# Optimization experiments

Measured on AMD Instinct MI355X. Metric: run time of the kernel, lower is better.

The kernel has to match this reference:

```python
import jax, jax.numpy as jnp
import numpy as np

START = 5.0
STEP = 8
SIZE = 256
STOP = SIZE // 2 - 1.0  # self.stop = int(size/2) - 1.0
# Original loops over tf.linspace(s, stop, step) and truncates each value to int.
US = [int(v) for v in np.linspace(START, STOP, STEP)]


def _block_mask(w, h, u):
    # Boolean block of ones of size (2u+1)^2 centered at (w//2, h//2).
    # Original: dd[half_w-u:half_w+u+1, half_h-u:half_h+u+1] = 1, then keeps
    # only that region of the shifted spectrum (ideal low-pass filter).
    m = np.zeros((w, h), dtype=np.float32)
    m[w // 2 - u: w // 2 + u + 1, h // 2 - u: h // 2 + u + 1] = 1.0
    return jnp.asarray(m)


def setup_inputs() -> dict:
    key = jax.random.key(0)
    x = jax.random.normal(key, (64, SIZE, SIZE, 1), dtype=jnp.float32)
    return {"x": x}


def reference(x):
    n, w, h, c = x.shape  # c == 1
    im = x[..., 0].astype(jnp.complex64)  # [n, w, h]
    # FFT is identical across loop iterations in the original; hoist it.
    # fftshift/ifftshift over all axes in TF cancel on the batch axis, so
    # shifting only the spatial axes is mathematically identical.
    freq = jnp.fft.fftshift(jnp.fft.fft2(im), axes=(-2, -1))
    outs = [x]
    for u in US:  # small fixed loop over STEP cutoff radii
        mask = _block_mask(w, h, u)
        low = freq * mask.astype(jnp.complex64)  # keep low frequencies only
        out = jnp.real(jnp.fft.ifft2(jnp.fft.ifftshift(low, axes=(-2, -1))))
        outs.append(out.astype(x.dtype)[..., None])
    return jnp.concatenate(outs, axis=-1)  # [n, w, h, STEP+1]
```

## Files before the change

kernel.cpp:

```cpp
#include <hip/hip_runtime.h>

typedef __attribute__((ext_vector_type(4))) float          f32x4;
typedef __attribute__((ext_vector_type(2))) float          f32x2;
typedef __attribute__((ext_vector_type(4))) unsigned int   u32x4;
typedef __attribute__((ext_vector_type(4))) unsigned short u16x4;
typedef __attribute__((ext_vector_type(2))) unsigned short u16x2;

typedef const unsigned int __attribute__((address_space(1)))* gas_ptr;
typedef unsigned int __attribute__((address_space(3)))*       las_ptr;

#define PI_F 3.14159265358979f

__device__ __forceinline__ unsigned short f2bf(float f) {
    unsigned int x = __float_as_uint(f);
    unsigned int r = ((x >> 16) & 1u) + 0x7fffu;
    return (unsigned short)((x + r) >> 16);
}
__device__ __forceinline__ float bf2f(unsigned short v) {
    return __uint_as_float((unsigned int)v << 16);
}
__device__ __forceinline__ void mfma16(f32x4& c, u32x4 a, u32x4 b) {
    asm volatile("v_mfma_f32_16x16x32_bf16 %0, %1, %2, %0"
                 : "+v"(c) : "v"(a), "v"(b));
}
__device__ __forceinline__ void gload16(const void* g, void* l) {
    __builtin_amdgcn_global_load_lds((gas_ptr)g, (las_ptr)l, 16, 0, 0);
}

#define SWZ(r, cb) (((unsigned)(r) * 128u) + ((unsigned)(cb) ^ ((((unsigned)(r)) & 7u) << 4)))

__global__ void prep(const float* __restrict__ x, unsigned short* __restrict__ H,
                     unsigned short* __restrict__ Xb, float* __restrict__ out,
                     int write_c0) {
    int b = blockIdx.x;
    if (b < 2048) {
        const int US[8] = {5, 22, 39, 57, 74, 92, 109, 127};
        int idx = b * 256 + threadIdx.x;
        int u = idx >> 16;
        int i = (idx >> 8) & 255, js = idx & 255;
        int jl = js ^ ((i & 7) << 3);
        int d = (i - jl) & 255;
        int m = 2 * US[u] + 1;
        float h;
        if (d == 0) {
            h = (float)m * (1.0f / 256.0f);
        } else {
            int t = (m * d) & 511;
            float num = sinf((float)t * (PI_F / 256.0f));
            float den = sinf((float)d * (PI_F / 256.0f));
            h = num / (256.0f * den);
        }
        H[idx] = f2bf(h);
    } else {
        int idx = (b - 2048) * 256 + threadIdx.x;
        f32x4 v = ((const f32x4*)x)[idx];
        u16x4 o = { f2bf(v.x), f2bf(v.y), f2bf(v.z), f2bf(v.w) };
        int n = idx >> 14;
        int t = idx & 16383;
        int i = t >> 6;
        int jlin = (t & 63) * 4;
        int js = jlin ^ ((i & 7) << 3);
        *(u16x4*)(Xb + (size_t)n * 65536 + i * 256 + js) = o;
        if (write_c0) {
            size_t g = (size_t)idx * 4;
            out[(g + 0) * 9] = v.x;
            out[(g + 1) * 9] = v.y;
            out[(g + 2) * 9] = v.z;
            out[(g + 3) * 9] = v.w;
        }
    }
}

__global__ void __launch_bounds__(256) stage12(const unsigned short* __restrict__ Xb,
                                               const unsigned short* __restrict__ H,
                                               unsigned short* __restrict__ Zb,
                                               float* __restrict__ fOut,
                                               int mode, int u_fixed) {
    extern __shared__ char smem[];
    char* sStage = smem;
    char* sHq    = smem + 32768;
    char* sT     = smem + 40960;

    int n, u, jq;
    if (u_fixed >= 0) {
        n = blockIdx.x >> 2; jq = blockIdx.x & 3; u = u_fixed;
    } else {
        int swz = (blockIdx.x & 7) * 256 + (blockIdx.x >> 3);
        n = swz >> 5; u = (swz >> 2) & 7; jq = swz & 3;
    }

    const char* Xn = (const char*)(Xb + (size_t)n * 65536);
    const char* Hu = (const char*)(H + (size_t)u * 65536);

    const int tid  = threadIdx.x;
    const int lane = tid & 63;
    const int w    = tid >> 6;
    const int lrow = lane & 15;
    const int lk   = lane >> 4;
    const int srow = lane >> 3, sch = lane & 7;

    f32x4 acc[4][4];
#pragma unroll
    for (int a = 0; a < 4; ++a)
#pragma unroll
        for (int b = 0; b < 4; ++b) acc[a][b] = (f32x4){0.f, 0.f, 0.f, 0.f};

    for (int kt = 0; kt < 4; ++kt) {
        if (kt) __syncthreads();
#pragma unroll
        for (int q = 0; q < 8; ++q) {
            int r = (w * 8 + q) * 8 + srow;
            gload16(Xn + r * 512 + kt * 128 + sch * 16, sStage + (w * 8 + q) * 1024);
        }
#pragma unroll
        for (int q = 0; q < 2; ++q) {
            int r = jq * 64 + (w * 2 + q) * 8 + srow;
            gload16(Hu + r * 512 + kt * 128 + sch * 16, sHq + (w * 2 + q) * 1024);
        }
        __syncthreads();
#pragma unroll
        for (int kk = 0; kk < 2; ++kk) {
            const int kb = kk * 64 + lk * 16;
            u32x4 af[4], bf[4];
#pragma unroll
            for (int mi = 0; mi < 4; ++mi)
                af[mi] = *(const u32x4*)(sStage + SWZ(w * 64 + mi * 16 + lrow, kb));
#pragma unroll
            for (int ni = 0; ni < 4; ++ni)
                bf[ni] = *(const u32x4*)(sHq + SWZ(ni * 16 + lrow, kb));
#pragma unroll
            for (int mi = 0; mi < 4; ++mi)
#pragma unroll
                for (int ni = 0; ni < 4; ++ni)
                    mfma16(acc[mi][ni], af[mi], bf[ni]);
        }
    }
    asm volatile("s_nop 7\n\ts_nop 7");

#pragma unroll
    for (int mi = 0; mi < 4; ++mi) {
        int i4 = w * 64 + mi * 16 + (lane >> 4) * 4;
#pragma unroll
        for (int ni = 0; ni < 4; ++ni) {
            int jl = ni * 16 + lrow;
            u16x4 o = { f2bf(acc[mi][ni].x), f2bf(acc[mi][ni].y),
                        f2bf(acc[mi][ni].z), f2bf(acc[mi][ni].w) };
            *(u16x4*)(sT + jl * 512 + ((2 * i4) ^ ((jl & 7) << 4))) = o;
        }
    }
    __syncthreads();

#pragma unroll
    for (int a = 0; a < 4; ++a)
#pragma unroll
        for (int b = 0; b < 4; ++b) acc[a][b] = (f32x4){0.f, 0.f, 0.f, 0.f};

    for (int kt = 0; kt < 4; ++kt) {
        if (kt) __syncthreads();
#pragma unroll
        for (int q = 0; q < 8; ++q) {
            int r = (w * 8 + q) * 8 + srow;
            gload16(Hu + r * 512 + kt * 128 + sch * 16, sStage + (w * 8 + q) * 1024);
        }
        __syncthreads();
#pragma unroll
        for (int kk = 0; kk < 2; ++kk) {
            const int kb  = kk * 64 + lk * 16;
            const int kbT = kt * 128 + kb;
            u32x4 af[4], bf[4];
#pragma unroll
            for (int mi = 0; mi < 4; ++mi) {
                int r = mi * 16 + lrow;
                af[mi] = *(const u32x4*)(sT + r * 512 + (kbT ^ ((r & 7) << 4)));
            }
#pragma unroll
            for (int ni = 0; ni < 4; ++ni)
                bf[ni] = *(const u32x4*)(sStage + SWZ(w * 64 + ni * 16 + lrow, kb));
#pragma unroll
            for (int mi = 0; mi < 4; ++mi)
#pragma unroll
                for (int ni = 0; ni < 4; ++ni)
                    mfma16(acc[mi][ni], af[mi], bf[ni]);
        }
    }
    asm volatile("s_nop 7\n\ts_nop 7");

    if (mode == 0) {
        unsigned short* Op = Zb + ((size_t)(u * 64 + n)) * 65536 + jq * 64;
#pragma unroll
        for (int mi = 0; mi < 4; ++mi) {
            int r4 = mi * 16 + (lane >> 4) * 4;
#pragma unroll
            for (int ni = 0; ni < 4; ++ni) {
                int c = w * 64 + ni * 16 + lrow;
                u16x4 o = { f2bf(acc[mi][ni].x), f2bf(acc[mi][ni].y),
                            f2bf(acc[mi][ni].z), f2bf(acc[mi][ni].w) };
                *(u16x4*)(Op + (size_t)c * 256 + r4) = o;
            }
        }
    } else {
#pragma unroll
        for (int mi = 0; mi < 4; ++mi) {
            int r4 = mi * 16 + (lane >> 4) * 4;
#pragma unroll
            for (int ni = 0; ni < 4; ++ni) {
                int c = w * 64 + ni * 16 + lrow;
                float* o = fOut + (((size_t)n * 256 + c) * 256 + jq * 64 + r4) * 9 + 1 + u;
                o[0]  = acc[mi][ni].x;
                o[9]  = acc[mi][ni].y;
                o[18] = acc[mi][ni].z;
                o[27] = acc[mi][ni].w;
            }
        }
    }
}

__global__ void __launch_bounds__(256) pack9(const float* __restrict__ x,
                                             const unsigned short* __restrict__ Zb,
                                             float* __restrict__ out) {
    __shared__ float sl[9216];
    const int t = threadIdx.x;
    const size_t g0 = (size_t)blockIdx.x * 1024;

#pragma unroll
    for (int c = 0; c < 2; ++c) {
        int q = c * 512 + t * 2;
        size_t p = g0 + q;
        f32x2 xv = *(const f32x2*)(x + p);
        sl[q * 9]       = xv.x;
        sl[(q + 1) * 9] = xv.y;
#pragma unroll
        for (int u = 0; u < 8; ++u) {
            u16x2 z = *(const u16x2*)(Zb + (size_t)u * 4194304 + p);
            sl[q * 9 + 1 + u]       = bf2f(z.x);
            sl[(q + 1) * 9 + 1 + u] = bf2f(z.y);
        }
    }
    __syncthreads();
    float* ob = out + g0 * 9;
#pragma unroll
    for (int r = 0; r < 9; ++r) {
        int d = r * 1024 + t * 4;
        *(f32x4*)(ob + d) = *(const f32x4*)&sl[d];
    }
}

extern "C" void kernel_launch(void* const* d_in, const int* in_sizes, int n_in,
                              void* d_out, int out_size, void* d_ws, size_t ws_size,
                              hipStream_t stream) {
    const float* x = (const float*)d_in[0];
    float* out = (float*)d_out;
    char* ws = (char*)d_ws;

    unsigned short* H  = (unsigned short*)(ws);
    unsigned short* Xb = (unsigned short*)(ws + 1048576);
    unsigned short* Zb = (unsigned short*)(ws + 9437184);

    const size_t NEED_FULL = 76546048ull;
    const size_t LDS_BYTES = 73728;

    if (ws_size >= NEED_FULL) {
        prep<<<6144, 256, 0, stream>>>(x, H, Xb, out, 0);
        stage12<<<2048, 256, LDS_BYTES, stream>>>(Xb, H, Zb, nullptr, 0, -1);
        pack9<<<4096, 256, 0, stream>>>(x, Zb, out);
    } else {
        prep<<<6144, 256, 0, stream>>>(x, H, Xb, out, 1);
        for (int u = 0; u < 8; ++u)
            stage12<<<256, 256, LDS_BYTES, stream>>>(Xb, H, nullptr, out, 1, u);
    }
}
```

Before: 96.54 us.

## Load MFMA operands directly from global memory instead of LDS staging

Removes the global_load_lds staging of the X and H tiles into shared memory, along with the syncthreads around it, and reads MFMA fragments straight from global memory using the pre-swizzled layout. Only the transpose buffer stays in LDS, which cuts LDS use from 72KB to 32KB and should allow more blocks per CU. The cost is more global and L2 traffic, since each wave now fetches its own fragments without sharing them through LDS, and the 16-byte reads are scattered.

```diff
diff --git a/kernel.cpp b/kernel.cpp
--- a/kernel.cpp
+++ b/kernel.cpp
@@ -6,9 +6,6 @@
 typedef __attribute__((ext_vector_type(4))) unsigned short u16x4;
 typedef __attribute__((ext_vector_type(2))) unsigned short u16x2;
 
-typedef const unsigned int __attribute__((address_space(1)))* gas_ptr;
-typedef unsigned int __attribute__((address_space(3)))*       las_ptr;
-
 #define PI_F 3.14159265358979f
 
 __device__ __forceinline__ unsigned short f2bf(float f) {
@@ -23,11 +20,7 @@
     asm volatile("v_mfma_f32_16x16x32_bf16 %0, %1, %2, %0"
                  : "+v"(c) : "v"(a), "v"(b));
 }
-__device__ __forceinline__ void gload16(const void* g, void* l) {
-    __builtin_amdgcn_global_load_lds((gas_ptr)g, (las_ptr)l, 16, 0, 0);
-}
-
-#define SWZ(r, cb) (((unsigned)(r) * 128u) + ((unsigned)(cb) ^ ((((unsigned)(r)) & 7u) << 4)))
+
 
 __global__ void prep(const float* __restrict__ x, unsigned short* __restrict__ H,
                      unsigned short* __restrict__ Xb, float* __restrict__ out,
@@ -76,10 +69,7 @@
                                                unsigned short* __restrict__ Zb,
                                                float* __restrict__ fOut,
                                                int mode, int u_fixed) {
-    extern __shared__ char smem[];
-    char* sStage = smem;
-    char* sHq    = smem + 32768;
-    char* sT     = smem + 40960;
+    __shared__ char sT[32768];
 
     int n, u, jq;
     if (u_fixed >= 0) {
@@ -97,7 +87,9 @@
     const int w    = tid >> 6;
     const int lrow = lane & 15;
     const int lk   = lane >> 4;
-    const int srow = lane >> 3, sch = lane & 7;
+    const int lmask = (lrow & 7) << 4;
+    const int offk0 = (lk * 16) ^ lmask;
+    const int offk1 = (64 + lk * 16) ^ lmask;
 
     f32x4 acc[4][4];
 #pragma unroll
@@ -105,29 +97,18 @@
 #pragma unroll
         for (int b = 0; b < 4; ++b) acc[a][b] = (f32x4){0.f, 0.f, 0.f, 0.f};
 
+#pragma unroll
     for (int kt = 0; kt < 4; ++kt) {
-        if (kt) __syncthreads();
-#pragma unroll
-        for (int q = 0; q < 8; ++q) {
-            int r = (w * 8 + q) * 8 + srow;
-            gload16(Xn + r * 512 + kt * 128 + sch * 16, sStage + (w * 8 + q) * 1024);
-        }
-#pragma unroll
-        for (int q = 0; q < 2; ++q) {
-            int r = jq * 64 + (w * 2 + q) * 8 + srow;
-            gload16(Hu + r * 512 + kt * 128 + sch * 16, sHq + (w * 2 + q) * 1024);
-        }
-        __syncthreads();
 #pragma unroll
         for (int kk = 0; kk < 2; ++kk) {
-            const int kb = kk * 64 + lk * 16;
+            const int off = kt * 128 + (kk ? offk1 : offk0);
             u32x4 af[4], bf[4];
 #pragma unroll
             for (int mi = 0; mi < 4; ++mi)
-                af[mi] = *(const u32x4*)(sStage + SWZ(w * 64 + mi * 16 + lrow, kb));
+                af[mi] = *(const u32x4*)(Xn + (w * 64 + mi * 16 + lrow) * 512 + off);
 #pragma unroll
             for (int ni = 0; ni < 4; ++ni)
-                bf[ni] = *(const u32x4*)(sHq + SWZ(ni * 16 + lrow, kb));
+                bf[ni] = *(const u32x4*)(Hu + (jq * 64 + ni * 16 + lrow) * 512 + off);
 #pragma unroll
             for (int mi = 0; mi < 4; ++mi)
 #pragma unroll
@@ -155,27 +136,18 @@
 #pragma unroll
         for (int b = 0; b < 4; ++b) acc[a][b] = (f32x4){0.f, 0.f, 0.f, 0.f};
 
+#pragma unroll
     for (int kt = 0; kt < 4; ++kt) {
-        if (kt) __syncthreads();
-#pragma unroll
-        for (int q = 0; q < 8; ++q) {
-            int r = (w * 8 + q) * 8 + srow;
-            gload16(Hu + r * 512 + kt * 128 + sch * 16, sStage + (w * 8 + q) * 1024);
-        }
-        __syncthreads();
 #pragma unroll
         for (int kk = 0; kk < 2; ++kk) {
-            const int kb  = kk * 64 + lk * 16;
-            const int kbT = kt * 128 + kb;
+            const int off = kt * 128 + (kk ? offk1 : offk0);
             u32x4 af[4], bf[4];
 #pragma unroll
-            for (int mi = 0; mi < 4; ++mi) {
-                int r = mi * 16 + lrow;
-                af[mi] = *(const u32x4*)(sT + r * 512 + (kbT ^ ((r & 7) << 4)));
-            }
+            for (int mi = 0; mi < 4; ++mi)
+                af[mi] = *(const u32x4*)(sT + (mi * 16 + lrow) * 512 + off);
 #pragma unroll
             for (int ni = 0; ni < 4; ++ni)
-                bf[ni] = *(const u32x4*)(sStage + SWZ(w * 64 + ni * 16 + lrow, kb));
+                bf[ni] = *(const u32x4*)(Hu + (w * 64 + ni * 16 + lrow) * 512 + off);
 #pragma unroll
             for (int mi = 0; mi < 4; ++mi)
 #pragma unroll
@@ -257,15 +229,14 @@
     unsigned short* Zb = (unsigned short*)(ws + 9437184);
 
     const size_t NEED_FULL = 76546048ull;
-    const size_t LDS_BYTES = 73728;
 
     if (ws_size >= NEED_FULL) {
         prep<<<6144, 256, 0, stream>>>(x, H, Xb, out, 0);
-        stage12<<<2048, 256, LDS_BYTES, stream>>>(Xb, H, Zb, nullptr, 0, -1);
+        stage12<<<2048, 256, 0, stream>>>(Xb, H, Zb, nullptr, 0, -1);
         pack9<<<4096, 256, 0, stream>>>(x, Zb, out);
     } else {
         prep<<<6144, 256, 0, stream>>>(x, H, Xb, out, 1);
         for (int u = 0; u < 8; ++u)
-            stage12<<<256, 256, LDS_BYTES, stream>>>(Xb, H, nullptr, out, 1, u);
-    }
-}
+            stage12<<<256, 256, 0, stream>>>(Xb, H, nullptr, out, 1, u);
+    }
+}
```

Result: slower. 104.3 us (+8.0%).

## Compute u=127 low-pass output analytically from Nyquist row/column sums

Applied to the files above, without the earlier changes.

For the largest cutoff u=127, the block mask keeps every frequency except the Nyquist row and column. The output is therefore x minus a correction built from alternating-sign row sums, column sums and a total. prep gains 64 blocks that compute these sums, stage12 drops the u=127 GEMM work (1792 blocks instead of 2048), and pack9 rebuilds channel 8 in fp32 from x and the sums. This removes one eighth of the matmul work and also computes that channel at full precision instead of bf16. The new reduction blocks add a strided read of x and a small workspace buffer.

```diff
diff --git a/kernel.cpp b/kernel.cpp
--- a/kernel.cpp
+++ b/kernel.cpp
@@ -31,7 +31,7 @@
 
 __global__ void prep(const float* __restrict__ x, unsigned short* __restrict__ H,
                      unsigned short* __restrict__ Xb, float* __restrict__ out,
-                     int write_c0) {
+                     float* __restrict__ abc_out, int write_c0) {
     int b = blockIdx.x;
     if (b < 2048) {
         const int US[8] = {5, 22, 39, 57, 74, 92, 109, 127};
@@ -51,7 +51,7 @@
             h = num / (256.0f * den);
         }
         H[idx] = f2bf(h);
-    } else {
+    } else if (b < 6144) {
         int idx = (b - 2048) * 256 + threadIdx.x;
         f32x4 v = ((const f32x4*)x)[idx];
         u16x4 o = { f2bf(v.x), f2bf(v.y), f2bf(v.z), f2bf(v.w) };
@@ -68,6 +68,28 @@
             out[(g + 2) * 9] = v.z;
             out[(g + 3) * 9] = v.w;
         }
+    } else {
+        __shared__ float cw[4];
+        int n = b - 6144, t = threadIdx.x;
+        int w = t >> 6, lane = t & 63;
+        const float* xi = x + (size_t)n * 65536;
+        float sa = 0.f;
+        for (int i = 0; i < 256; ++i) {
+            float v = xi[i * 256 + t];
+            sa += (i & 1) ? -v : v;
+        }
+        float sb = 0.f;
+        for (int jb = 0; jb < 64; ++jb) {
+            f32x4 v4 = *(const f32x4*)(xi + t * 256 + jb * 4);
+            sb += (v4.x - v4.y) + (v4.z - v4.w);
+        }
+        abc_out[n * 768 + t]       = sa;
+        abc_out[n * 768 + 256 + t] = sb;
+        float sc = (t & 1) ? -sb : sb;
+        for (int off = 32; off; off >>= 1) sc += __shfl_down(sc, off);
+        if (lane == 0) cw[w] = sc;
+        __syncthreads();
+        if (t == 0) abc_out[n * 768 + 512] = cw[0] + cw[1] + cw[2] + cw[3];
     }
 }
 
@@ -85,8 +107,10 @@
     if (u_fixed >= 0) {
         n = blockIdx.x >> 2; jq = blockIdx.x & 3; u = u_fixed;
     } else {
-        int swz = (blockIdx.x & 7) * 256 + (blockIdx.x >> 3);
-        n = swz >> 5; u = (swz >> 2) & 7; jq = swz & 3;
+        int swz = (blockIdx.x & 7) * 224 + (blockIdx.x >> 3);
+        n = swz / 28;
+        int rr = swz - n * 28;
+        u = rr >> 2; jq = rr & 3;
     }
 
     const char* Xn = (const char*)(Xb + (size_t)n * 65536);
@@ -217,24 +241,37 @@
 
 __global__ void __launch_bounds__(256) pack9(const float* __restrict__ x,
                                              const unsigned short* __restrict__ Zb,
+                                             const float* __restrict__ abc_in,
                                              float* __restrict__ out) {
     __shared__ float sl[9216];
     const int t = threadIdx.x;
     const size_t g0 = (size_t)blockIdx.x * 1024;
+    const int n = (int)(g0 >> 16);
+    const float* ab = abc_in + n * 768;
+    const float cc = ab[512];
 
 #pragma unroll
     for (int c = 0; c < 2; ++c) {
         int q = c * 512 + t * 2;
         size_t p = g0 + q;
+        int j = (int)(p & 255);
+        int i = (int)((p >> 8) & 255);
         f32x2 xv = *(const f32x2*)(x + p);
         sl[q * 9]       = xv.x;
         sl[(q + 1) * 9] = xv.y;
 #pragma unroll
-        for (int u = 0; u < 8; ++u) {
+        for (int u = 0; u < 7; ++u) {
             u16x2 z = *(const u16x2*)(Zb + (size_t)u * 4194304 + p);
             sl[q * 9 + 1 + u]       = bf2f(z.x);
             sl[(q + 1) * 9 + 1 + u] = bf2f(z.y);
         }
+        float vi  = (i & 1) ? -1.f : 1.f;
+        f32x2 aj  = *(const f32x2*)(ab + j);
+        float bi  = ab[256 + i];
+        float z8a = xv.x - (vi * aj.x + bi) * (1.0f / 256.0f) + cc * vi * (1.0f / 65536.0f);
+        float z8b = xv.y - (vi * aj.y - bi) * (1.0f / 256.0f) - cc * vi * (1.0f / 65536.0f);
+        sl[q * 9 + 8]       = z8a;
+        sl[(q + 1) * 9 + 8] = z8b;
     }
     __syncthreads();
     float* ob = out + g0 * 9;
@@ -252,19 +289,20 @@
     float* out = (float*)d_out;
     char* ws = (char*)d_ws;
 
-    unsigned short* H  = (unsigned short*)(ws);
-    unsigned short* Xb = (unsigned short*)(ws + 1048576);
-    unsigned short* Zb = (unsigned short*)(ws + 9437184);
+    unsigned short* H    = (unsigned short*)(ws);
+    unsigned short* Xb   = (unsigned short*)(ws + 1048576);
+    unsigned short* Zb   = (unsigned short*)(ws + 9437184);
+    float*          abcb = (float*)(ws + 68157440);
 
     const size_t NEED_FULL = 76546048ull;
     const size_t LDS_BYTES = 73728;
 
     if (ws_size >= NEED_FULL) {
-        prep<<<6144, 256, 0, stream>>>(x, H, Xb, out, 0);
-        stage12<<<2048, 256, LDS_BYTES, stream>>>(Xb, H, Zb, nullptr, 0, -1);
-        pack9<<<4096, 256, 0, stream>>>(x, Zb, out);
+        prep<<<6208, 256, 0, stream>>>(x, H, Xb, out, abcb, 0);
+        stage12<<<1792, 256, LDS_BYTES, stream>>>(Xb, H, Zb, nullptr, 0, -1);
+        pack9<<<4096, 256, 0, stream>>>(x, Zb, abcb, out);
     } else {
-        prep<<<6144, 256, 0, stream>>>(x, H, Xb, out, 1);
+        prep<<<6144, 256, 0, stream>>>(x, H, Xb, out, nullptr, 1);
         for (int u = 0; u < 8; ++u)
             stage12<<<256, 256, LDS_BYTES, stream>>>(Xb, H, nullptr, out, 1, u);
     }
```

Measured after the change: 110.0 us. +14.0%, slower.
